# Optimization experiments

Measured on AMD Instinct MI355X. Metric: run time of the kernel, lower is better.

Reference implementation:

```python
import jax, jax.numpy as jnp
import numpy as np

SD = 64      # state_dim
EMO = 16     # emo_dim
D = SD + EMO # fractal node dim
C = SD       # quantum in/out channels
E = SD * 5   # MHA embed dim (320)
NH = 4       # MHA heads
HD = E // NH
F = D * 5    # flattened fractal node state
LIGHT = 500.0


def setup_inputs() -> dict:
    key = jax.random.key(0)
    ks = iter(jax.random.split(key, 48))
    def n(shape, s=0.02):
        return jax.random.normal(next(ks), shape, dtype=jnp.float32) * s
    return dict(
        node_states=jax.random.normal(next(ks), (27, SD, 5), dtype=jnp.float32),
        hist_state=jax.random.normal(next(ks), (27, SD, 5), dtype=jnp.float32),
        # CausalDiscoveryLayer params
        granger_W=n((2 * SD * 5, 1)), granger_b=jnp.zeros((1,), jnp.float32),
        mha_in_W=n((3 * E, E)), mha_in_b=jnp.zeros((3 * E,), jnp.float32),
        mha_out_W=n((E, E)), mha_out_b=jnp.zeros((E,), jnp.float32),
        # QuantumEntangledGNN params
        q_real=n((27, C), 0.01), q_imag=n((27, C), 0.01),
        ent_W1=n((2 * C, 64)), ent_b1=jnp.zeros((64,), jnp.float32),
        ent_W2=n((64, C)), ent_b2=jnp.zeros((C,), jnp.float32),
        meas_W=n((2 * C, C * 5)), meas_b=jnp.zeros((C * 5,), jnp.float32),
        # FractalGNN (depth 2, 27-ary): 729 leaves, 27 mid, 1 root
        leaf_states=n((729, D, 5), 0.01),
        mid_states=n((27, D, 5), 0.01),
        root_state=n((D, 5), 0.01),
        mid_agg_W=n((27, 27 * F, F)), mid_agg_b=jnp.zeros((27, F), jnp.float32),
        root_agg_W=n((27 * F, F)), root_agg_b=jnp.zeros((F,), jnp.float32),
        mid_up_W1=n((27, 2 * F, 64)), mid_up_b1=jnp.zeros((27, 64), jnp.float32),
        mid_up_W2=n((27, 64, F)), mid_up_b2=jnp.zeros((27, F), jnp.float32),
        root_up_W1=n((2 * F, 64)), root_up_b1=jnp.zeros((64,), jnp.float32),
        root_up_W2=n((64, F)), root_up_b2=jnp.zeros((F,), jnp.float32),
    )


def _forward(node_states, hist_state, granger_W, granger_b, mha_in_W, mha_in_b,
             mha_out_W, mha_out_b, q_real, q_imag, ent_W1, ent_b1, ent_W2, ent_b2,
             meas_W, meas_b, leaf_states, mid_states, root_state, mid_agg_W,
             mid_agg_b, root_agg_W, root_agg_b, mid_up_W1, mid_up_b1, mid_up_W2,
             mid_up_b2, root_up_W1, root_up_b1, root_up_W2, root_up_b2):
    # ---- CausalDiscoveryLayer ----
    h = hist_state.reshape(27, SD * 5)   # historical_states[-1][j].view(-1)
    x = node_states.reshape(27, SD * 5)  # node_states[i].view(-1)
    # pred_input[i, j] = cat(hist[j], node[i]) -> granger test, all 27x27 pairs
    pred = jnp.concatenate([
        jnp.broadcast_to(h[None, :, :], (27, 27, SD * 5)),
        jnp.broadcast_to(x[:, None, :], (27, 27, SD * 5))], axis=-1)
    scores = jax.nn.sigmoid(pred @ granger_W + granger_b)[..., 0]
    # .item() in original detaches -> stop_gradient; diagonal stays zero
    causal_adj = jax.lax.stop_gradient(scores * (1.0 - jnp.eye(27, dtype=scores.dtype)))
    hertz_w = jnp.clip(jnp.float32(LIGHT / 1000.0), 0.1, 1.0)
    qkv = x @ mha_in_W.T + mha_in_b
    q, k, v = jnp.split(qkv, 3, axis=-1)
    qh = q.reshape(27, NH, HD).transpose(1, 0, 2)  # [h, s, d]
    kh = k.reshape(27, NH, HD).transpose(1, 0, 2)
    vh = v.reshape(27, NH, HD).transpose(1, 0, 2)
    attn = jax.nn.softmax(jnp.einsum('hqd,hkd->hqk', qh, kh) / jnp.float32(HD) ** 0.5, axis=-1)
    o = jnp.einsum('hqk,hkd->hqd', attn, vh).transpose(1, 0, 2).reshape(27, E)
    attended = ((o @ mha_out_W.T + mha_out_b) * hertz_w).reshape(27, SD, 5)

    # ---- QuantumEntangledGNN (351 unordered pairs i<j) ----
    iu, ju = np.triu_indices(27, 1)
    comb = jnp.concatenate([q_real[iu], q_real[ju]], axis=-1)       # [351, 2C]
    ent = jax.nn.relu(comb @ ent_W1 + ent_b1) @ ent_W2 + ent_b2     # [351, C]
    s = q_real.sum(axis=1)
    coupling = jnp.exp(-jnp.abs(s[iu] - s[ju]) / (LIGHT + 1e-6))
    avg_ent = (ent * coupling[:, None]).mean(axis=0)                # [C]
    qr = q_real + avg_ent[None, :]
    qi = q_imag + avg_ent[None, :]
    measured = (jnp.concatenate([qr, qi], axis=-1) @ meas_W + meas_b).reshape(3, 3, 3, C, 5)

    # ---- FractalGNN: leaves are passthrough; 27 mid nodes update, then root ----
    child_flat = leaf_states.reshape(27, 27 * F)  # each mid node's 27 leaf children
    agg = jnp.einsum('nij,ni->nj', mid_agg_W, child_flat) + mid_agg_b  # [27, F]
    comb_m = jnp.concatenate([mid_states.reshape(27, F), agg], axis=-1)
    hid = jax.nn.relu(jnp.einsum('nij,ni->nj', mid_up_W1, comb_m) + mid_up_b1)
    upd = jnp.einsum('nij,ni->nj', mid_up_W2, hid) + mid_up_b2
    new_mid = mid_states + upd.reshape(27, D, 5)
    cf = new_mid.reshape(27 * F)
    agg_r = cf @ root_agg_W + root_agg_b
    comb_r = jnp.concatenate([root_state.reshape(F), agg_r], axis=-1)
    new_root = root_state + (jax.nn.relu(comb_r @ root_up_W1 + root_up_b1) @ root_up_W2 + root_up_b2).reshape(D, 5)

    return causal_adj, attended, measured, new_root


def reference(node_states, hist_state, granger_W, granger_b, mha_in_W, mha_in_b,
              mha_out_W, mha_out_b, q_real, q_imag, ent_W1, ent_b1, ent_W2, ent_b2,
              meas_W, meas_b, leaf_states, mid_states, root_state, mid_agg_W,
              mid_agg_b, root_agg_W, root_agg_b, mid_up_W1, mid_up_b1, mid_up_W2,
              mid_up_b2, root_up_W1, root_up_b1, root_up_W2, root_up_b2):
    return _forward(node_states, hist_state, granger_W, granger_b, mha_in_W,
                    mha_in_b, mha_out_W, mha_out_b, q_real, q_imag, ent_W1, ent_b1,
                    ent_W2, ent_b2, meas_W, meas_b, leaf_states, mid_states,
                    root_state, mid_agg_W, mid_agg_b, root_agg_W, root_agg_b,
                    mid_up_W1, mid_up_b1, mid_up_W2, mid_up_b2, root_up_W1,
                    root_up_b1, root_up_W2, root_up_b2)
```

## Files before the change

### kernel.cpp

```cpp
#include <hip/hip_runtime.h>
#include <math.h>

typedef float v4f __attribute__((ext_vector_type(4)));

#define SD 64
#define CC 64
#define EE 320
#define NS 27
#define NPAIR 351

#define NCHUNK 27
#define AGG_BLKS (27 * NCHUNK)
#define NRCHUNK 216

#define WS_QKV   0
#define WS_ENT   25920
#define WS_MIDP  48384
#define WS_CF    339984
#define WS_ROOTP 350784
#define WS_HPM   437184
#define WS_CTR   444096
#define WS_O     444128
#define WS_AVG   452768


__device__ void dev_mid_agg(int blk, const float* __restrict__ W,
                            const float* __restrict__ leaf, float* __restrict__ partial) {
    __shared__ float c_l[400];
    __shared__ __align__(16) float racc[5][400];
    int n = blk / NCHUNK, chunk = blk % NCHUNK;
    int t = threadIdx.x;
    if (t < 400) c_l[t] = leaf[n * 10800 + chunk * 400 + t];
    __syncthreads();
    if (t < 500) {
        int rp = t / 100, j4 = t % 100;
        const v4f* pA = (const v4f*)(W + (size_t)(n * 10800 + chunk * 400) * 400) + rp * 100 + j4;
        const v4f* pB = pA + 500;
        v4f a0 = (v4f)(0.0f), a1 = (v4f)(0.0f);
        #pragma unroll 8
        for (int rr = 0; rr < 40; ++rr) {
            v4f wa = __builtin_nontemporal_load(pA);
            v4f wb = __builtin_nontemporal_load(pB);
            a0 += c_l[10 * rr + rp] * wa;
            a1 += c_l[10 * rr + rp + 5] * wb;
            pA += 1000; pB += 1000;
        }
        a0 += a1;
        ((v4f*)&racc[rp][0])[j4] = a0;
    }
    __syncthreads();
    if (t < 400) {
        float a = racc[0][t] + racc[1][t] + racc[2][t] + racc[3][t] + racc[4][t];
        partial[(size_t)blk * 400 + t] = a;
    }
}

__device__ void dev_granger(int blk, const float* __restrict__ x, const float* __restrict__ h,
                            const float* __restrict__ gW, const float* __restrict__ gb,
                            float* __restrict__ out) {
    int idx = blk * 512 + threadIdx.x;
    if (idx >= NS * NS) return;
    int i = idx / NS, j = idx % NS;
    const float* hr = h + j * 320;
    const float* xr = x + i * 320;
    float acc = gb[0];
    for (int k = 0; k < 320; ++k) acc += hr[k] * gW[k] + xr[k] * gW[320 + k];
    float sig = 1.0f / (1.0f + expf(-acc));
    out[idx] = (i == j) ? 0.0f : sig;
}

__device__ void dev_qkv(int blk, const float* __restrict__ x, const float* __restrict__ W,
                        const float* __restrict__ b, float* __restrict__ qkv) {
    int idx = blk * 512 + threadIdx.x;
    if (idx >= NS * 960) return;
    int i = idx / 960, c = idx % 960;
    const float4* xr = (const float4*)(x + i * 320);
    const float4* wr = (const float4*)(W + (size_t)c * 320);
    float acc = b[c];
    #pragma unroll 8
    for (int k = 0; k < 80; ++k) {
        float4 a = xr[k], w = wr[k];
        acc += a.x * w.x + a.y * w.y + a.z * w.z + a.w * w.w;
    }
    qkv[idx] = acc;
}

__device__ void dev_ent(int blk, const float* __restrict__ q_real,
                        const float* __restrict__ W1, const float* __restrict__ b1,
                        const float* __restrict__ W2, const float* __restrict__ b2,
                        float* __restrict__ ent_scaled) {
    __shared__ float comb[4][128];
    __shared__ float hid[4][64];
    int t = threadIdx.x;
    int sub = t >> 7, lt = t & 127;
    int p = blk * 4 + sub;
    bool pv = (p < NPAIR);
    bool valid = pv && (lt < 64);
    int i = 0, jj = 0;
    if (pv) {
        int rem = p;
        while (rem >= 26 - i) { rem -= 26 - i; ++i; }
        jj = i + 1 + rem;
    }
    float qa = 0.f, qb = 0.f;
    if (valid) { qa = q_real[i * CC + lt]; qb = q_real[jj * CC + lt]; }
    float sa = qa, sb = qb;
    #pragma unroll
    for (int off = 32; off; off >>= 1) { sa += __shfl_xor(sa, off); sb += __shfl_xor(sb, off); }
    float coupling = expf(-fabsf(sa - sb) / (500.0f + 1e-6f));
    if (valid) { comb[sub][lt] = qa; comb[sub][64 + lt] = qb; }
    __syncthreads();
    if (valid) {
        float hs = b1[lt];
        for (int ii = 0; ii < 128; ++ii) hs += comb[sub][ii] * W1[ii * 64 + lt];
        hid[sub][lt] = fmaxf(hs, 0.0f);
    }
    __syncthreads();
    if (valid) {
        float e = b2[lt];
        for (int k = 0; k < 64; ++k) e += hid[sub][k] * W2[k * 64 + lt];
        ent_scaled[p * 64 + lt] = e * coupling;
    }
}

__global__ __launch_bounds__(512) void k_stage1(
    const float* __restrict__ mid_agg_W, const float* __restrict__ leaf,
    const float* __restrict__ node, const float* __restrict__ hist,
    const float* __restrict__ gW, const float* __restrict__ gb,
    const float* __restrict__ mha_in_W, const float* __restrict__ mha_in_b,
    const float* __restrict__ q_real,
    const float* __restrict__ ent_W1, const float* __restrict__ ent_b1,
    const float* __restrict__ ent_W2, const float* __restrict__ ent_b2,
    float* __restrict__ mid_partial, float* __restrict__ out_causal,
    float* __restrict__ qkv, float* __restrict__ ent_scaled,
    int* __restrict__ ctrs) {
    int blk = blockIdx.x;
    if (blk == 0 && threadIdx.x >= 480) ctrs[threadIdx.x - 480] = 0;
    if (blk < AGG_BLKS)           dev_mid_agg(blk, mid_agg_W, leaf, mid_partial);
    else if (blk < AGG_BLKS + 2)  dev_granger(blk - AGG_BLKS, node, hist, gW, gb, out_causal);
    else if (blk < AGG_BLKS + 53) dev_qkv(blk - AGG_BLKS - 2, node, mha_in_W, mha_in_b, qkv);
    else                          dev_ent(blk - AGG_BLKS - 53, q_real, ent_W1, ent_b1, ent_W2, ent_b2, ent_scaled);
}


__device__ void dev_attn(int blk, const float* __restrict__ qkv, float* __restrict__ o) {
    int h = blk / NS, q = blk % NS;
    int t = threadIdx.x;
    __shared__ float sc[NS];
    __shared__ float at[NS];
    if (t < NS) {
        const float* qrow = qkv + q * 960 + h * 80;
        const float* krow = qkv + t * 960 + EE + h * 80;
        float s = 0.0f;
        for (int d = 0; d < 80; ++d) s += qrow[d] * krow[d];
        sc[t] = s * 0.1118033988749895f;
    }
    __syncthreads();
    if (t < NS) {
        float m = -1e30f;
        for (int s2 = 0; s2 < NS; ++s2) m = fmaxf(m, sc[s2]);
        float sum = 0.0f;
        for (int s2 = 0; s2 < NS; ++s2) sum += expf(sc[s2] - m);
        at[t] = expf(sc[t] - m) / sum;
    }
    __syncthreads();
    if (t < 80) {
        float acc = 0.0f;
        for (int s2 = 0; s2 < NS; ++s2) acc += at[s2] * qkv[s2 * 960 + 2 * EE + h * 80 + t];
        o[q * EE + h * 80 + t] = acc;
    }
}

__device__ void dev_avg(const float* __restrict__ ent_scaled, float* __restrict__ avg) {
    __shared__ float aacc[8][64];
    int t = threadIdx.x;
    int col = t & 63, grp = t >> 6;
    float s = 0.0f;
    for (int p = grp; p < NPAIR; p += 8) s += ent_scaled[p * 64 + col];
    aacc[grp][col] = s;
    __syncthreads();
    if (t < 64) {
        float a = 0.0f;
        #pragma unroll
        for (int g = 0; g < 8; ++g) a += aacc[g][t];
        avg[t] = a / (float)NPAIR;
    }
}

__device__ void dev_mid_up(int rel, const float* __restrict__ partial, const float* __restrict__ agg_b,
                           const float* __restrict__ mid_states,
                           const float* __restrict__ W1, const float* __restrict__ b1,
                           const float* __restrict__ W2, const float* __restrict__ b2,
                           float* __restrict__ cf, float* __restrict__ hpm, int* __restrict__ ctrs) {
    int n = rel >> 2, p = rel & 3;
    __shared__ float combq[200];
    __shared__ float hp8[8][64];
    __shared__ float hid[64];
    __shared__ int flag;
    int t = threadIdx.x;
    if (p < 2) {
        if (t < 200) combq[t] = mid_states[n * 400 + p * 200 + t];
    } else {
        int j0 = (p - 2) * 200;
        if (t < 200) {
            float a = agg_b[n * 400 + j0 + t];
            const float* pp = partial + (size_t)(n * NCHUNK) * 400 + j0 + t;
            #pragma unroll 9
            for (int s = 0; s < NCHUNK; ++s) a += pp[s * 400];
            combq[t] = a;
        }
    }
    __syncthreads();
    {
        int h = t & 63, g = t >> 6;
        const float* w1 = W1 + (size_t)n * 51200 + (size_t)(p * 200) * 64;
        float hs = 0.0f;
        #pragma unroll 5
        for (int i = g * 25; i < g * 25 + 25; ++i) hs += combq[i] * w1[i * 64 + h];
        hp8[g][h] = hs;
    }
    __syncthreads();
    if (t < 64) {
        float hs = 0.0f;
        #pragma unroll
        for (int g = 0; g < 8; ++g) hs += hp8[g][t];
        hpm[(n * 4 + p) * 64 + t] = hs;
    }
    __syncthreads();
    if (t == 0) {
        int old = __hip_atomic_fetch_add(&ctrs[n], 1, __ATOMIC_ACQ_REL, __HIP_MEMORY_SCOPE_AGENT);
        flag = (old == 3);
    }
    __syncthreads();
    if (flag) {
        if (t < 64) {
            float hs = b1[n * 64 + t];
            #pragma unroll
            for (int pq = 0; pq < 4; ++pq) hs += hpm[(n * 4 + pq) * 64 + t];
            hid[t] = fmaxf(hs, 0.0f);
        }
        __syncthreads();
        const float* w2 = W2 + (size_t)n * 25600;
        if (t < 400) {
            float u = b2[n * 400 + t];
            #pragma unroll 8
            for (int k = 0; k < 64; ++k) u += hid[k] * w2[k * 400 + t];
            cf[n * 400 + t] = mid_states[n * 400 + t] + u;
        }
    }
}

__global__ __launch_bounds__(512) void k_stage2(
    const float* __restrict__ qkv, float* __restrict__ o,
    const float* __restrict__ ent_scaled, float* __restrict__ avg,
    const float* __restrict__ mid_partial, const float* __restrict__ mid_agg_b,
    const float* __restrict__ mid_states,
    const float* __restrict__ mid_up_W1, const float* __restrict__ mid_up_b1,
    const float* __restrict__ mid_up_W2, const float* __restrict__ mid_up_b2,
    float* __restrict__ cf, float* __restrict__ hpm, int* __restrict__ ctrs) {
    int blk = blockIdx.x;
    if (blk < 108)       dev_attn(blk, qkv, o);
    else if (blk == 108) dev_avg(ent_scaled, avg);
    else                 dev_mid_up(blk - 109, mid_partial, mid_agg_b, mid_states,
                                    mid_up_W1, mid_up_b1, mid_up_W2, mid_up_b2, cf, hpm, ctrs);
}


__device__ void dev_proj(int blk, const float* __restrict__ o, const float* __restrict__ W,
                         const float* __restrict__ b, float* __restrict__ outp) {
    int idx = blk * 512 + threadIdx.x;
    if (idx >= NS * EE) return;
    int i = idx / EE, c = idx % EE;
    const float4* orow = (const float4*)(o + i * EE);
    const float4* wr = (const float4*)(W + (size_t)c * EE);
    float acc = b[c];
    #pragma unroll 8
    for (int k = 0; k < 80; ++k) {
        float4 a = orow[k], w = wr[k];
        acc += a.x * w.x + a.y * w.y + a.z * w.z + a.w * w.w;
    }
    outp[idx] = 0.5f * acc;
}

__device__ void dev_measured(int blk, const float* __restrict__ q_real, const float* __restrict__ q_imag,
                             const float* __restrict__ avg, const float* __restrict__ W,
                             const float* __restrict__ b, float* __restrict__ out) {
    int idx = blk * 512 + threadIdx.x;
    if (idx >= NS * EE) return;
    int i = idx / EE, c = idx % EE;
    float acc = b[c];
    #pragma unroll 8
    for (int k = 0; k < 64; ++k) {
        float a = avg[k];
        acc += (q_real[i * 64 + k] + a) * W[k * EE + c];
        acc += (q_imag[i * 64 + k] + a) * W[(64 + k) * EE + c];
    }
    out[idx] = acc;
}

__device__ void dev_rootagg(int chunk, const float* __restrict__ W, const float* __restrict__ cf,
                            float* __restrict__ partial_r,
                            const float* __restrict__ agg_b, const float* __restrict__ root_state,
                            const float* __restrict__ W1, const float* __restrict__ b1,
                            const float* __restrict__ W2, const float* __restrict__ b2,
                            float* __restrict__ out, int* __restrict__ ctrs) {
    __shared__ float c_l[50];
    __shared__ __align__(16) float racc[5][400];
    __shared__ int flag;
    int t = threadIdx.x;
    if (t < 50) c_l[t] = cf[chunk * 50 + t];
    __syncthreads();
    if (t < 500) {
        int rp = t / 100, j4 = t % 100;
        const v4f* pA = (const v4f*)W + (size_t)(chunk * 50) * 100 + rp * 100 + j4;
        const v4f* pB = pA + 500;
        v4f a0 = (v4f)(0.0f), a1 = (v4f)(0.0f);
        #pragma unroll
        for (int rr = 0; rr < 5; ++rr) {
            v4f wa = __builtin_nontemporal_load(pA);
            v4f wb = __builtin_nontemporal_load(pB);
            a0 += c_l[10 * rr + rp] * wa;
            a1 += c_l[10 * rr + rp + 5] * wb;
            pA += 1000; pB += 1000;
        }
        a0 += a1;
        ((v4f*)&racc[rp][0])[j4] = a0;
    }
    __syncthreads();
    if (t < 400) {
        float a = racc[0][t] + racc[1][t] + racc[2][t] + racc[3][t] + racc[4][t];
        partial_r[chunk * 400 + t] = a;
    }
    __syncthreads();
    if (t == 0) {
        int old = __hip_atomic_fetch_add(&ctrs[31], 1, __ATOMIC_ACQ_REL, __HIP_MEMORY_SCOPE_AGENT);
        flag = (old == NRCHUNK - 1);
    }
    __syncthreads();
    if (!flag) return;

    __shared__ float comb[800];
    __shared__ __align__(16) float s4f[2048];
    __shared__ float hid[64];
    if (t < 400) {
        float a = agg_b[t];
        const float* pp = partial_r + t;
        #pragma unroll 8
        for (int s = 0; s < NRCHUNK; ++s) a += pp[s * 400];
        comb[400 + t] = a;
        comb[t] = root_state[t];
    }
    __syncthreads();
    {
        const float4* W1f = (const float4*)W1;
        int i0 = t >> 4;
        float4 a4 = make_float4(0.f, 0.f, 0.f, 0.f);
        #pragma unroll
        for (int it = 0; it < 25; ++it) {
            float4 w = W1f[t + 512 * it];
            float cv = comb[i0 + 32 * it];
            a4.x += cv * w.x; a4.y += cv * w.y; a4.z += cv * w.z; a4.w += cv * w.w;
        }
        ((float4*)s4f)[t] = a4;
    }
    __syncthreads();
    if (t < 64) {
        float hs = b1[t];
        int r = t >> 2, c = t & 3;
        #pragma unroll 8
        for (int g = 0; g < 32; ++g) hs += s4f[(r + 16 * g) * 4 + c];
        hid[t] = fmaxf(hs, 0.0f);
    }
    __syncthreads();
    if (t < 400) {
        float u = b2[t];
        #pragma unroll 8
        for (int k = 0; k < 64; ++k) u += hid[k] * W2[k * 400 + t];
        out[t] = root_state[t] + u;
    }
}

__global__ __launch_bounds__(512) void k_stage3(
    const float* __restrict__ o, const float* __restrict__ mha_out_W,
    const float* __restrict__ mha_out_b, float* __restrict__ out_att,
    const float* __restrict__ q_real, const float* __restrict__ q_imag,
    const float* __restrict__ avg, const float* __restrict__ meas_W,
    const float* __restrict__ meas_b, float* __restrict__ out_meas,
    const float* __restrict__ root_agg_W, const float* __restrict__ cf,
    float* __restrict__ partial_r,
    const float* __restrict__ root_agg_b, const float* __restrict__ root_state,
    const float* __restrict__ root_up_W1, const float* __restrict__ root_up_b1,
    const float* __restrict__ root_up_W2, const float* __restrict__ root_up_b2,
    float* __restrict__ out_root, int* __restrict__ ctrs) {
    int blk = blockIdx.x;
    if (blk < 17)       dev_proj(blk, o, mha_out_W, mha_out_b, out_att);
    else if (blk < 34)  dev_measured(blk - 17, q_real, q_imag, avg, meas_W, meas_b, out_meas);
    else                dev_rootagg(blk - 34, root_agg_W, cf, partial_r,
                                    root_agg_b, root_state, root_up_W1, root_up_b1,
                                    root_up_W2, root_up_b2, out_root, ctrs);
}

extern "C" void kernel_launch(void* const* d_in, const int* in_sizes, int n_in,
                              void* d_out, int out_size, void* d_ws, size_t ws_size,
                              hipStream_t stream) {
    const float* node       = (const float*)d_in[0];
    const float* hist       = (const float*)d_in[1];
    const float* gW         = (const float*)d_in[2];
    const float* gb         = (const float*)d_in[3];
    const float* mha_in_W   = (const float*)d_in[4];
    const float* mha_in_b   = (const float*)d_in[5];
    const float* mha_out_W  = (const float*)d_in[6];
    const float* mha_out_b  = (const float*)d_in[7];
    const float* q_real     = (const float*)d_in[8];
    const float* q_imag     = (const float*)d_in[9];
    const float* ent_W1     = (const float*)d_in[10];
    const float* ent_b1     = (const float*)d_in[11];
    const float* ent_W2     = (const float*)d_in[12];
    const float* ent_b2     = (const float*)d_in[13];
    const float* meas_W     = (const float*)d_in[14];
    const float* meas_b     = (const float*)d_in[15];
    const float* leaf       = (const float*)d_in[16];
    const float* mid_states = (const float*)d_in[17];
    const float* root_state = (const float*)d_in[18];
    const float* mid_agg_W  = (const float*)d_in[19];
    const float* mid_agg_b  = (const float*)d_in[20];
    const float* root_agg_W = (const float*)d_in[21];
    const float* root_agg_b = (const float*)d_in[22];
    const float* mid_up_W1  = (const float*)d_in[23];
    const float* mid_up_b1  = (const float*)d_in[24];
    const float* mid_up_W2  = (const float*)d_in[25];
    const float* mid_up_b2  = (const float*)d_in[26];
    const float* root_up_W1 = (const float*)d_in[27];
    const float* root_up_b1 = (const float*)d_in[28];
    const float* root_up_W2 = (const float*)d_in[29];
    const float* root_up_b2 = (const float*)d_in[30];

    float* ws          = (float*)d_ws;
    float* qkv         = ws + WS_QKV;
    float* ent_scaled  = ws + WS_ENT;
    float* mid_partial = ws + WS_MIDP;
    float* cf          = ws + WS_CF;
    float* partial_r   = ws + WS_ROOTP;
    float* hpm         = ws + WS_HPM;
    int*   ctrs        = (int*)(ws + WS_CTR);
    float* o           = ws + WS_O;
    float* avg         = ws + WS_AVG;

    float* out        = (float*)d_out;
    float* out_causal = out;
    float* out_att    = out + 729;
    float* out_meas   = out + 9369;
    float* out_root   = out + 18009;

    hipLaunchKernelGGL(k_stage1, dim3(AGG_BLKS + 2 + 51 + 88), dim3(512), 0, stream,
                       mid_agg_W, leaf, node, hist, gW, gb, mha_in_W, mha_in_b,
                       q_real, ent_W1, ent_b1, ent_W2, ent_b2,
                       mid_partial, out_causal, qkv, ent_scaled, ctrs);

    hipLaunchKernelGGL(k_stage2, dim3(217), dim3(512), 0, stream,
                       qkv, o, ent_scaled, avg, mid_partial, mid_agg_b, mid_states,
                       mid_up_W1, mid_up_b1, mid_up_W2, mid_up_b2, cf, hpm, ctrs);

    hipLaunchKernelGGL(k_stage3, dim3(250), dim3(512), 0, stream,
                       o, mha_out_W, mha_out_b, out_att,
                       q_real, q_imag, avg, meas_W, meas_b, out_meas,
                       root_agg_W, cf, partial_r,
                       root_agg_b, root_state, root_up_W1, root_up_b1,
                       root_up_W2, root_up_b2, out_root, ctrs);
}
```

Baseline: 144.2 us.

## Stream mid-aggregation weights through double-buffered LDS with async global-to-LDS loads

After: 153.1 us. 6.2% more time.

```diff
diff --git a/kernel.cpp b/kernel.cpp
--- a/kernel.cpp
+++ b/kernel.cpp
@@ -23,36 +23,43 @@
 #define WS_O     444128
 #define WS_AVG   452768
 
+__device__ __forceinline__ void gload_lds16(const float* g, float* l) {
+    __builtin_amdgcn_global_load_lds(
+        (const __attribute__((address_space(1))) unsigned int*)(g),
+        (__attribute__((address_space(3))) unsigned int*)(l),
+        16, 0, 0);
+}
+
 
 __device__ void dev_mid_agg(int blk, const float* __restrict__ W,
                             const float* __restrict__ leaf, float* __restrict__ partial) {
     __shared__ float c_l[400];
-    __shared__ __align__(16) float racc[5][400];
+    __shared__ __align__(16) float Wl[2][6400];
+    int t = threadIdx.x;
     int n = blk / NCHUNK, chunk = blk % NCHUNK;
-    int t = threadIdx.x;
+    int wv = t >> 6, lane = t & 63;
+    const float* Wg = W + (size_t)(n * 10800 + chunk * 400) * 400;
     if (t < 400) c_l[t] = leaf[n * 10800 + chunk * 400 + t];
-    __syncthreads();
-    if (t < 500) {
-        int rp = t / 100, j4 = t % 100;
-        const v4f* pA = (const v4f*)(W + (size_t)(n * 10800 + chunk * 400) * 400) + rp * 100 + j4;
-        const v4f* pB = pA + 500;
-        v4f a0 = (v4f)(0.0f), a1 = (v4f)(0.0f);
-        #pragma unroll 8
-        for (int rr = 0; rr < 40; ++rr) {
-            v4f wa = __builtin_nontemporal_load(pA);
-            v4f wb = __builtin_nontemporal_load(pB);
-            a0 += c_l[10 * rr + rp] * wa;
-            a1 += c_l[10 * rr + rp + 5] * wb;
-            pA += 1000; pB += 1000;
-        }
-        a0 += a1;
-        ((v4f*)&racc[rp][0])[j4] = a0;
-    }
-    __syncthreads();
-    if (t < 400) {
-        float a = racc[0][t] + racc[1][t] + racc[2][t] + racc[3][t] + racc[4][t];
-        partial[(size_t)blk * 400 + t] = a;
-    }
+    for (int c = wv; c < 25; c += 8)
+        gload_lds16(Wg + c * 256 + lane * 4, &Wl[0][c * 256]);
+    __syncthreads();
+    float acc = 0.0f;
+    int buf = 0;
+    for (int tile = 0; tile < 25; ++tile) {
+        if (tile < 24) {
+            const float* Wt = Wg + (size_t)(tile + 1) * 6400;
+            for (int c = wv; c < 25; c += 8)
+                gload_lds16(Wt + c * 256 + lane * 4, &Wl[buf ^ 1][c * 256]);
+        }
+        if (t < 400) {
+            #pragma unroll
+            for (int r = 0; r < 16; ++r)
+                acc += c_l[tile * 16 + r] * Wl[buf][r * 400 + t];
+        }
+        __syncthreads();
+        buf ^= 1;
+    }
+    if (t < 400) partial[(size_t)blk * 400 + t] = acc;
 }
 
 __device__ void dev_granger(int blk, const float* __restrict__ x, const float* __restrict__ h,
```
